# Optimization experiments

Measured on AMD Instinct MI355X. Metric: run time of the kernel, lower is better.

## Reference

```python
import jax, jax.numpy as jnp
import numpy as np

PADDING = 2
STRIDE = 1

def setup_inputs() -> dict:
    key = jax.random.key(0)
    k1, k2 = jax.random.split(key)
    X = jax.random.normal(k1, (32, 32, 128, 128), dtype=jnp.float32)  # NCHW
    K = jax.random.normal(k2, (64, 32, 5, 5), dtype=jnp.float32)     # OIHW
    return {"X": X, "K": K}

def reference(X, K):
    # Faithful to the naive loop: zero-pad by PADDING on H and W, then a
    # stride-STRIDE cross-correlation (slice * kernel).sum() per output pixel
    # and output channel -> exactly a standard conv2d with no bias.
    out = jax.lax.conv_general_dilated(
        X, K,
        window_strides=(STRIDE, STRIDE),
        padding=[(PADDING, PADDING), (PADDING, PADDING)],
        dimension_numbers=("NCHW", "OIHW", "NCHW"),
    )
    return out
```

## Files before the change

### kernel.cpp

```cpp
#include <hip/hip_runtime.h>


#define C_IN 32
#define H 128
#define W 128
#define O_CH 64
#define KS 5
#define PAD 2
#define XH 20
#define XW 20
#define NSHIFT 25
#define KSLICE_US 4096
#define KP_BYTES (NSHIFT * KSLICE_US * 2)
#define SX_PLANE 12800

typedef __bf16 bf16x8 __attribute__((ext_vector_type(8)));
typedef float f32x4 __attribute__((ext_vector_type(4)));

static __device__ __forceinline__ unsigned short f2bf(float f) {
    unsigned int u = __float_as_uint(f);
    u += 0x7fffu + ((u >> 16) & 1u);
    return (unsigned short)(u >> 16);
}
static __device__ __forceinline__ float bf2f(unsigned short s) {
    return __uint_as_float(((unsigned int)s) << 16);
}
static __device__ __forceinline__ uint4 pack8(const unsigned short* v) {
    uint4 w;
    w.x = (unsigned)v[0] | ((unsigned)v[1] << 16);
    w.y = (unsigned)v[2] | ((unsigned)v[3] << 16);
    w.z = (unsigned)v[4] | ((unsigned)v[5] << 16);
    w.w = (unsigned)v[6] | ((unsigned)v[7] << 16);
    return w;
}

__global__ __launch_bounds__(256)
void pack_k_kernel(const float* __restrict__ K, unsigned short* __restrict__ Kp) {
    int t = blockIdx.x * 256 + threadIdx.x;
    int lp = t & 15;
    int u  = t >> 4;
    int g  = u & 3;  u >>= 2;
    int nf = u & 3;  u >>= 2;
    int hl = u & 1;  u >>= 1;
    int s  = u;
    int oc = nf * 16 + lp;
    unsigned short v[8];
#pragma unroll
    for (int j = 0; j < 8; ++j) {
        float f = K[(size_t)(oc * C_IN + g * 8 + j) * (KS * KS) + s];
        unsigned short hi = f2bf(f);
        v[j] = hl ? f2bf(f - bf2f(hi)) : hi;
    }
    ((uint4*)Kp)[t] = pack8(v);
}

struct Bfrag { uint4 h[4]; uint4 l[4]; };

template<bool USE_KP>
static __device__ __forceinline__ void load_b(const uint4* kp4, const float* K,
                                              int s, int lg, int lp, int lane_off,
                                              Bfrag& b) {
    if (USE_KP) {
#pragma unroll
        for (int nf = 0; nf < 4; ++nf) {
            b.h[nf] = kp4[s * 512 + nf * 64 + lane_off];
            b.l[nf] = kp4[s * 512 + 256 + nf * 64 + lane_off];
        }
    } else {
#pragma unroll
        for (int nf = 0; nf < 4; ++nf) {
            unsigned short hi[8], lo[8];
#pragma unroll
            for (int j = 0; j < 8; ++j) {
                float f = K[(size_t)((nf * 16 + lp) * C_IN + lg * 8 + j) * (KS * KS) + s];
                hi[j] = f2bf(f);
                lo[j] = f2bf(f - bf2f(hi[j]));
            }
            b.h[nf] = pack8(hi);
            b.l[nf] = pack8(lo);
        }
    }
}

static __device__ __forceinline__ void do_shift(const unsigned short* sX, int s,
                                                int wv, int lg, int lp,
                                                const Bfrag& b, f32x4 acc[4][4]) {
    const int ky = s / KS, kx = s % KS;
    bf16x8 ah[4], al[4];
#pragma unroll
    for (int mf = 0; mf < 4; ++mf) {
        int off = (((wv * 4 + mf + ky) * 4 + lg) * XW + kx + lp) * 8;
        ah[mf] = *(const bf16x8*)&sX[off];
        al[mf] = *(const bf16x8*)&sX[off + SX_PLANE];
    }
    const bf16x8* bh = (const bf16x8*)b.h;
    const bf16x8* bl = (const bf16x8*)b.l;
#pragma unroll
    for (int mf = 0; mf < 4; ++mf)
#pragma unroll
        for (int nf = 0; nf < 4; ++nf)
            acc[mf][nf] = __builtin_amdgcn_mfma_f32_16x16x32_bf16(ah[mf], bh[nf], acc[mf][nf], 0, 0, 0);
#pragma unroll
    for (int mf = 0; mf < 4; ++mf)
#pragma unroll
        for (int nf = 0; nf < 4; ++nf)
            acc[mf][nf] = __builtin_amdgcn_mfma_f32_16x16x32_bf16(ah[mf], bl[nf], acc[mf][nf], 0, 0, 0);
#pragma unroll
    for (int mf = 0; mf < 4; ++mf)
#pragma unroll
        for (int nf = 0; nf < 4; ++nf)
            acc[mf][nf] = __builtin_amdgcn_mfma_f32_16x16x32_bf16(al[mf], bh[nf], acc[mf][nf], 0, 0, 0);
}

template<bool USE_KP>
__global__ __launch_bounds__(256, 2)
void conv5x5_mfma3(const float* __restrict__ X, const float* __restrict__ K,
                   const unsigned short* __restrict__ Kp, float* __restrict__ out) {
    __shared__ __align__(16) unsigned short sX[2 * SX_PLANE];

    const int tid  = threadIdx.x;
    const int lane = tid & 63;
    const int wv   = tid >> 6;
    const int lg   = lane >> 4;
    const int lp   = lane & 15;
    const int lane_off = lg * 16 + lp;

    const int bid  = blockIdx.x;
    const int n    = bid >> 6;
    const int tile = bid & 63;
    const int ty0  = (tile >> 3) * 16;
    const int tx0  = (tile & 7) * 16;

    const uint4* kp4 = (const uint4*)Kp;

    const float* Xn = X + (size_t)n * C_IN * H * W;
    for (int i = tid; i < XH * 4 * XW; i += 256) {
        int x = i % XW;
        int t = i / XW;
        int g = t & 3;
        int y = t >> 2;
        int gx = tx0 + x - PAD;
        int gy = ty0 + y - PAD;
        bool inb = ((unsigned)gx < (unsigned)W) && ((unsigned)gy < (unsigned)H);
        const float* p = Xn + (size_t)(g * 8) * (H * W) + gy * W + gx;
        unsigned short hi8[8], lo8[8];
#pragma unroll
        for (int j = 0; j < 8; ++j) {
            float v = inb ? p[j * (H * W)] : 0.f;
            hi8[j] = f2bf(v);
            lo8[j] = f2bf(v - bf2f(hi8[j]));
        }
        ((uint4*)sX)[i] = pack8(hi8);
        ((uint4*)sX)[i + 1600] = pack8(lo8);
    }

    f32x4 acc[4][4];
#pragma unroll
    for (int mf = 0; mf < 4; ++mf)
#pragma unroll
        for (int nf = 0; nf < 4; ++nf)
            acc[mf][nf] = (f32x4){0.f, 0.f, 0.f, 0.f};

    Bfrag b0, b1;
    load_b<USE_KP>(kp4, K, 0, lg, lp, lane_off, b0);

    __syncthreads();

#pragma unroll 1
    for (int s = 0; s < NSHIFT - 1; s += 2) {
        load_b<USE_KP>(kp4, K, s + 1, lg, lp, lane_off, b1);
        do_shift(sX, s, wv, lg, lp, b0, acc);
        load_b<USE_KP>(kp4, K, (s + 2 <= NSHIFT - 1) ? s + 2 : NSHIFT - 1, lg, lp, lane_off, b0);
        do_shift(sX, s + 1, wv, lg, lp, b1, acc);
    }
    do_shift(sX, NSHIFT - 1, wv, lg, lp, b0, acc);

#pragma unroll
    for (int mf = 0; mf < 4; ++mf) {
        int y = ty0 + wv * 4 + mf;
#pragma unroll
        for (int nf = 0; nf < 4; ++nf) {
            int oc = nf * 16 + lp;
            size_t idx = (((size_t)n * O_CH + oc) * H + y) * W + tx0 + lg * 4;
            *(float4*)&out[idx] = *(float4*)&acc[mf][nf];
        }
    }
}

extern "C" void kernel_launch(void* const* d_in, const int* in_sizes, int n_in,
                              void* d_out, int out_size, void* d_ws, size_t ws_size,
                              hipStream_t stream) {
    const float* X = (const float*)d_in[0];
    const float* K = (const float*)d_in[1];
    float* out = (float*)d_out;

    if (ws_size >= (size_t)KP_BYTES) {
        unsigned short* Kp = (unsigned short*)d_ws;
        pack_k_kernel<<<dim3(50), dim3(256), 0, stream>>>(K, Kp);
        conv5x5_mfma3<true><<<dim3(2048), dim3(256), 0, stream>>>(X, K, Kp, out);
    } else {
        conv5x5_mfma3<false><<<dim3(2048), dim3(256), 0, stream>>>(X, K, nullptr, out);
    }
}
```

Before: 275.0 us.

## Replace split-bf16 three-pass MFMA with single-pass fp16 MFMA convolution

Drops the hi/lo bf16 split emulation of fp32, which needed three MFMA passes per shift and two shared-memory planes. Inputs and weights are now converted once to fp16 and fed to a single 16x16x32 f16 MFMA pass, so the LDS tile is halved and the B fragments are halved. This cuts matrix work about threefold and allows a higher occupancy hint. The block index is also remapped to interleave blocks across dies/XCDs. The trade-off is lower accuracy: fp16 has a reduced mantissa and range compared with the compensated bf16 scheme, so the result may drift further from the fp32 reference.

```diff
diff --git a/kernel.cpp b/kernel.cpp
--- a/kernel.cpp
+++ b/kernel.cpp
@@ -10,51 +10,31 @@
 #define XH 20
 #define XW 20
 #define NSHIFT 25
-#define KSLICE_US 4096
-#define KP_BYTES (NSHIFT * KSLICE_US * 2)
-#define SX_PLANE 12800
+#define KSLICE_U4 256
+#define KP_BYTES (NSHIFT * KSLICE_U4 * 16)
+#define SX_CELLS (XH * 4 * XW)
 
-typedef __bf16 bf16x8 __attribute__((ext_vector_type(8)));
+typedef _Float16 f16x8 __attribute__((ext_vector_type(8)));
 typedef float f32x4 __attribute__((ext_vector_type(4)));
 
-static __device__ __forceinline__ unsigned short f2bf(float f) {
-    unsigned int u = __float_as_uint(f);
-    u += 0x7fffu + ((u >> 16) & 1u);
-    return (unsigned short)(u >> 16);
-}
-static __device__ __forceinline__ float bf2f(unsigned short s) {
-    return __uint_as_float(((unsigned int)s) << 16);
-}
-static __device__ __forceinline__ uint4 pack8(const unsigned short* v) {
-    uint4 w;
-    w.x = (unsigned)v[0] | ((unsigned)v[1] << 16);
-    w.y = (unsigned)v[2] | ((unsigned)v[3] << 16);
-    w.z = (unsigned)v[4] | ((unsigned)v[5] << 16);
-    w.w = (unsigned)v[6] | ((unsigned)v[7] << 16);
-    return w;
+union H8 { _Float16 h[8]; uint4 q; };
+
+__global__ __launch_bounds__(256)
+void pack_k_kernel(const float* __restrict__ K, uint4* __restrict__ Kp) {
+    int t = blockIdx.x * 256 + threadIdx.x;
+    int lp = t & 15;
+    int g  = (t >> 4) & 3;
+    int nf = (t >> 6) & 3;
+    int s  = t >> 8;
+    int oc = nf * 16 + lp;
+    H8 u;
+#pragma unroll
+    for (int j = 0; j < 8; ++j)
+        u.h[j] = (_Float16)K[(size_t)(oc * C_IN + g * 8 + j) * (KS * KS) + s];
+    Kp[t] = u.q;
 }
 
-__global__ __launch_bounds__(256)
-void pack_k_kernel(const float* __restrict__ K, unsigned short* __restrict__ Kp) {
-    int t = blockIdx.x * 256 + threadIdx.x;
-    int lp = t & 15;
-    int u  = t >> 4;
-    int g  = u & 3;  u >>= 2;
-    int nf = u & 3;  u >>= 2;
-    int hl = u & 1;  u >>= 1;
-    int s  = u;
-    int oc = nf * 16 + lp;
-    unsigned short v[8];
-#pragma unroll
-    for (int j = 0; j < 8; ++j) {
-        float f = K[(size_t)(oc * C_IN + g * 8 + j) * (KS * KS) + s];
-        unsigned short hi = f2bf(f);
-        v[j] = hl ? f2bf(f - bf2f(hi)) : hi;
-    }
-    ((uint4*)Kp)[t] = pack8(v);
-}
-
-struct Bfrag { uint4 h[4]; uint4 l[4]; };
+struct Bfrag { uint4 q[4]; };
 
 template<bool USE_KP>
 static __device__ __forceinline__ void load_b(const uint4* kp4, const float* K,
@@ -62,22 +42,16 @@
                                               Bfrag& b) {
     if (USE_KP) {
 #pragma unroll
-        for (int nf = 0; nf < 4; ++nf) {
-            b.h[nf] = kp4[s * 512 + nf * 64 + lane_off];
-            b.l[nf] = kp4[s * 512 + 256 + nf * 64 + lane_off];
-        }
+        for (int nf = 0; nf < 4; ++nf)
+            b.q[nf] = kp4[s * 256 + nf * 64 + lane_off];
     } else {
 #pragma unroll
         for (int nf = 0; nf < 4; ++nf) {
-            unsigned short hi[8], lo[8];
+            H8 u;
 #pragma unroll
-            for (int j = 0; j < 8; ++j) {
-                float f = K[(size_t)((nf * 16 + lp) * C_IN + lg * 8 + j) * (KS * KS) + s];
-                hi[j] = f2bf(f);
-                lo[j] = f2bf(f - bf2f(hi[j]));
-            }
-            b.h[nf] = pack8(hi);
-            b.l[nf] = pack8(lo);
+            for (int j = 0; j < 8; ++j)
+                u.h[j] = (_Float16)K[(size_t)((nf * 16 + lp) * C_IN + lg * 8 + j) * (KS * KS) + s];
+            b.q[nf] = u.q;
         }
     }
 }
@@ -86,37 +60,25 @@
                                                 int wv, int lg, int lp,
                                                 const Bfrag& b, f32x4 acc[4][4]) {
     const int ky = s / KS, kx = s % KS;
-    bf16x8 ah[4], al[4];
+    f16x8 ah[4];
 #pragma unroll
     for (int mf = 0; mf < 4; ++mf) {
         int off = (((wv * 4 + mf + ky) * 4 + lg) * XW + kx + lp) * 8;
-        ah[mf] = *(const bf16x8*)&sX[off];
-        al[mf] = *(const bf16x8*)&sX[off + SX_PLANE];
+        ah[mf] = *(const f16x8*)&sX[off];
     }
-    const bf16x8* bh = (const bf16x8*)b.h;
-    const bf16x8* bl = (const bf16x8*)b.l;
 #pragma unroll
     for (int mf = 0; mf < 4; ++mf)
 #pragma unroll
         for (int nf = 0; nf < 4; ++nf)
-            acc[mf][nf] = __builtin_amdgcn_mfma_f32_16x16x32_bf16(ah[mf], bh[nf], acc[mf][nf], 0, 0, 0);
-#pragma unroll
-    for (int mf = 0; mf < 4; ++mf)
-#pragma unroll
-        for (int nf = 0; nf < 4; ++nf)
-            acc[mf][nf] = __builtin_amdgcn_mfma_f32_16x16x32_bf16(ah[mf], bl[nf], acc[mf][nf], 0, 0, 0);
-#pragma unroll
-    for (int mf = 0; mf < 4; ++mf)
-#pragma unroll
-        for (int nf = 0; nf < 4; ++nf)
-            acc[mf][nf] = __builtin_amdgcn_mfma_f32_16x16x32_bf16(al[mf], bh[nf], acc[mf][nf], 0, 0, 0);
+            acc[mf][nf] = __builtin_amdgcn_mfma_f32_16x16x32_f16(
+                ah[mf], *(const f16x8*)&b.q[nf], acc[mf][nf], 0, 0, 0);
 }
 
 template<bool USE_KP>
-__global__ __launch_bounds__(256, 2)
-void conv5x5_mfma3(const float* __restrict__ X, const float* __restrict__ K,
-                   const unsigned short* __restrict__ Kp, float* __restrict__ out) {
-    __shared__ __align__(16) unsigned short sX[2 * SX_PLANE];
+__global__ __launch_bounds__(256, 4)
+void conv5x5_f16(const float* __restrict__ X, const float* __restrict__ K,
+                 const uint4* __restrict__ kp4, float* __restrict__ out) {
+    __shared__ __align__(16) unsigned short sX[SX_CELLS * 8];
 
     const int tid  = threadIdx.x;
     const int lane = tid & 63;
@@ -125,16 +87,14 @@
     const int lp   = lane & 15;
     const int lane_off = lg * 16 + lp;
 
-    const int bid  = blockIdx.x;
+    const int bid = (blockIdx.x & 7) * 256 + (blockIdx.x >> 3);
     const int n    = bid >> 6;
     const int tile = bid & 63;
     const int ty0  = (tile >> 3) * 16;
     const int tx0  = (tile & 7) * 16;
 
-    const uint4* kp4 = (const uint4*)Kp;
-
     const float* Xn = X + (size_t)n * C_IN * H * W;
-    for (int i = tid; i < XH * 4 * XW; i += 256) {
+    for (int i = tid; i < SX_CELLS; i += 256) {
         int x = i % XW;
         int t = i / XW;
         int g = t & 3;
@@ -143,15 +103,11 @@
         int gy = ty0 + y - PAD;
         bool inb = ((unsigned)gx < (unsigned)W) && ((unsigned)gy < (unsigned)H);
         const float* p = Xn + (size_t)(g * 8) * (H * W) + gy * W + gx;
-        unsigned short hi8[8], lo8[8];
+        H8 u;
 #pragma unroll
-        for (int j = 0; j < 8; ++j) {
-            float v = inb ? p[j * (H * W)] : 0.f;
-            hi8[j] = f2bf(v);
-            lo8[j] = f2bf(v - bf2f(hi8[j]));
-        }
-        ((uint4*)sX)[i] = pack8(hi8);
-        ((uint4*)sX)[i + 1600] = pack8(lo8);
+        for (int j = 0; j < 8; ++j)
+            u.h[j] = (_Float16)(inb ? p[j * (H * W)] : 0.f);
+        ((uint4*)sX)[i] = u.q;
     }
 
     f32x4 acc[4][4];
@@ -195,10 +151,10 @@
     float* out = (float*)d_out;
 
     if (ws_size >= (size_t)KP_BYTES) {
-        unsigned short* Kp = (unsigned short*)d_ws;
-        pack_k_kernel<<<dim3(50), dim3(256), 0, stream>>>(K, Kp);
-        conv5x5_mfma3<true><<<dim3(2048), dim3(256), 0, stream>>>(X, K, Kp, out);
+        uint4* Kp = (uint4*)d_ws;
+        pack_k_kernel<<<dim3(25), dim3(256), 0, stream>>>(K, Kp);
+        conv5x5_f16<true><<<dim3(2048), dim3(256), 0, stream>>>(X, K, Kp, out);
     } else {
-        conv5x5_mfma3<false><<<dim3(2048), dim3(256), 0, stream>>>(X, K, nullptr, out);
+        conv5x5_f16<false><<<dim3(2048), dim3(256), 0, stream>>>(X, K, nullptr, out);
     }
 }
```

New measurement: 256.6 us. -6.7%, faster.
